# Kernel optimization log

Measured on AMD Instinct MI355X. Metric: run time of the kernel, lower is better.

The kernel has to match this reference:

```python
import jax, jax.numpy as jnp
import numpy as np

T, B, I, H = 256, 128, 512, 1024

def setup_inputs() -> dict:
    key = jax.random.key(0)
    k1, k2, k3, k4, k5 = jax.random.split(key, 5)
    s_ih = 1.0 / np.sqrt(H)
    return {
        "x": jax.random.normal(k1, (T, B, I), dtype=jnp.float32),
        "hidden": jnp.zeros((B, H), dtype=jnp.float32),
        "W_ih": jax.random.uniform(k2, (H, I), jnp.float32, -s_ih, s_ih),
        "W_hh": jax.random.uniform(k3, (H, H), jnp.float32, -s_ih, s_ih),
        "b_ih": jax.random.uniform(k4, (H,), jnp.float32, -s_ih, s_ih),
        "b_hh": jax.random.uniform(k5, (H,), jnp.float32, -s_ih, s_ih),
    }

def reference(x, hidden, W_ih, W_hh, b_ih, b_hh):
    # Faithful to the source: forward() applies the RNNCell to the SAME
    # initial hidden at every timestep (hidden is never updated in the loop).
    # out[t] = relu(x[t] @ W_ih^T + b_ih + hidden @ W_hh^T + b_hh)
    h_term = hidden @ W_hh.T + b_hh          # (B, H), shared across time
    pre = jnp.einsum('tbi,hi->tbh', x, W_ih) + b_ih + h_term  # (T, B, H)
    out = jax.nn.relu(pre)
    return out, out[-1]
```

## Files before the change

### kernel.cpp

```cpp
#include <hip/hip_runtime.h>
#include <hip/hip_bf16.h>
#include <stdint.h>

#define T_DIM 256
#define B_DIM 128
#define I_DIM 512
#define H_DIM 1024
#define M_DIM (T_DIM * B_DIM)

typedef __attribute__((ext_vector_type(4))) float f32x4;
typedef __attribute__((ext_vector_type(8))) short short8;

__device__ inline unsigned short f2bf(float f) {
    __hip_bfloat16 h = __float2bfloat16(f);
    unsigned short u;
    __builtin_memcpy(&u, &h, sizeof(u));
    return u;
}

__device__ inline void gload_lds16(const void* g, void* l) {
    __builtin_amdgcn_global_load_lds(
        (const __attribute__((address_space(1))) uint32_t*)g,
        (__attribute__((address_space(3))) uint32_t*)l, 16, 0, 0);
}

__global__ void pack_swz(const float* __restrict__ src,
                         unsigned short* __restrict__ dst) {
    int id = blockIdx.x * 256 + threadIdx.x;
    int slot = id & 7;
    int row = (id >> 3) & 127;
    int kst = (id >> 10) & 7;
    int tile = id >> 13;
    int g = slot ^ (row & 7);
    const float* s = src + (size_t)(tile * 128 + row) * I_DIM + kst * 64 + g * 8;
    f32x4 lo = *(const f32x4*)s;
    f32x4 hi = *(const f32x4*)(s + 4);
    union { unsigned short us[8]; short8 v; } pk;
#pragma unroll
    for (int j = 0; j < 4; ++j) { pk.us[j] = f2bf(lo[j]); pk.us[4 + j] = f2bf(hi[j]); }
    *(short8*)(dst + (size_t)id * 8) = pk.v;
}

__global__ __launch_bounds__(256, 2) void gemm_main(
    const unsigned short* __restrict__ Xp, const unsigned short* __restrict__ Wp,
    const float* __restrict__ biasall, float* __restrict__ C,
    float* __restrict__ Clast) {
    __shared__ unsigned short As[2][128 * 64];
    __shared__ unsigned short Bs[2][128 * 64];

    const int tid = threadIdx.x;
    const int lane = tid & 63;
    const int wid = tid >> 6;
    const int wr = wid >> 1, wc = wid & 1;
    const int llo = lane & 15, lhi = lane >> 4;

    const int orig = blockIdx.x;
    const int wg = ((orig & 7) * (2048 >> 3)) + (orig >> 3);
    const int mt = wg >> 3;
    const int nt = wg & 7;
    const int m0 = mt * 128;
    const int n0 = nt * 128;

    const unsigned short* Abase = Xp + (size_t)mt * 65536 + (size_t)tid * 8;
    const unsigned short* Bbase = Wp + (size_t)nt * 65536 + (size_t)tid * 8;

    auto stage = [&](int kst, int buf) {
        const unsigned short* a = Abase + (size_t)kst * 8192;
        const unsigned short* b = Bbase + (size_t)kst * 8192;
#pragma unroll
        for (int g = 0; g < 4; ++g)
            gload_lds16(a + g * 2048, (char*)As[buf] + (g * 256 + tid) * 16);
#pragma unroll
        for (int g = 0; g < 4; ++g)
            gload_lds16(b + g * 2048, (char*)Bs[buf] + (g * 256 + tid) * 16);
    };

    f32x4 acc[4][4] = {};

    auto compute = [&](int buf) {
#pragma unroll
        for (int ks = 0; ks < 2; ++ks) {
            short8 af[4], bfv[4];
#pragma unroll
            for (int mi = 0; mi < 4; ++mi) {
                int ar = wr * 64 + mi * 16 + llo;
                int g = ks * 4 + lhi;
                af[mi] = *(const short8*)&As[buf][ar * 64 + ((g ^ (ar & 7)) << 3)];
            }
#pragma unroll
            for (int ni = 0; ni < 4; ++ni) {
                int br = wc * 64 + ni * 16 + llo;
                int g = ks * 4 + lhi;
                bfv[ni] = *(const short8*)&Bs[buf][br * 64 + ((g ^ (br & 7)) << 3)];
            }
#pragma unroll
            for (int mi = 0; mi < 4; ++mi)
#pragma unroll
                for (int ni = 0; ni < 4; ++ni)
                    acc[mi][ni] = __builtin_amdgcn_mfma_f32_16x16x32_bf16(
                        af[mi], bfv[ni], acc[mi][ni], 0, 0, 0);
        }
    };

    stage(0, 0);
    stage(1, 1);
#pragma unroll
    for (int k = 0; k < 8; ++k) {
        if (k < 7)
            asm volatile("s_waitcnt vmcnt(8)" ::: "memory");
        else
            asm volatile("s_waitcnt vmcnt(0)" ::: "memory");
        __builtin_amdgcn_s_barrier();
        __builtin_amdgcn_sched_barrier(0);
        compute(k & 1);
        __builtin_amdgcn_sched_barrier(0);
        __builtin_amdgcn_s_barrier();
        if (k + 2 < 8) stage(k + 2, k & 1);
    }

    const bool last_tile = (m0 == M_DIM - 128);
#pragma unroll
    for (int mi = 0; mi < 4; ++mi) {
#pragma unroll
        for (int ni = 0; ni < 4; ++ni) {
            int col = n0 + wc * 64 + ni * 16 + llo;
            int rowb = m0 + wr * 64 + mi * 16 + lhi * 4;
#pragma unroll
            for (int r = 0; r < 4; ++r) {
                int row = rowb + r;
                float v = acc[mi][ni][r] + biasall[(row & 127) * H_DIM + col];
                v = fmaxf(v, 0.0f);
                C[(size_t)row * H_DIM + col] = v;
                if (last_tile) Clast[(row & 127) * H_DIM + col] = v;
            }
        }
    }
}

template <int MODE>
__global__ __launch_bounds__(256, 2) void gemm_bt(
    const float* __restrict__ A, const float* __restrict__ Bm,
    int M, int N, int K,
    const float* __restrict__ bias0, const float* __restrict__ bias1,
    float* __restrict__ C, float* __restrict__ Clast) {
    __shared__ unsigned short As[128 * 64];
    __shared__ unsigned short Bs[128 * 64];

    const int tid = threadIdx.x;
    const int wid = tid >> 6;
    const int lane = tid & 63;
    const int wr = wid >> 1, wc = wid & 1;
    const int lhi = lane >> 4;
    const int llo = lane & 15;

    const int orig = blockIdx.x;
    const int nwg = gridDim.x;
    const int wg = (nwg > 8 && (nwg & 7) == 0)
                       ? ((orig & 7) * (nwg >> 3) + (orig >> 3))
                       : orig;
    const int m0 = (wg >> 3) * 128;
    const int n0 = (wg & 7) * 128;

    const int srow = tid >> 3;
    const int c8 = tid & 7;
    const int slot8 = (c8 ^ (srow & 7)) * 8;

    const float* Aptr = A + (size_t)(m0 + srow) * K + c8 * 8;
    const float* Bptr = Bm + (size_t)(n0 + srow) * K + c8 * 8;

    f32x4 pf[2][4][2];

    auto issue = [&](int k0) {
#pragma unroll
        for (int g = 0; g < 4; ++g) {
            const float* pa = Aptr + (size_t)g * 32 * K + k0;
            const float* pb = Bptr + (size_t)g * 32 * K + k0;
            pf[0][g][0] = *(const f32x4*)pa;
            pf[0][g][1] = *(const f32x4*)(pa + 4);
            pf[1][g][0] = *(const f32x4*)pb;
            pf[1][g][1] = *(const f32x4*)(pb + 4);
        }
    };
    auto write_lds = [&]() {
#pragma unroll
        for (int g = 0; g < 4; ++g) {
            union { unsigned short s[8]; short8 v; } pka, pkb;
#pragma unroll
            for (int j = 0; j < 4; ++j) {
                pka.s[j] = f2bf(pf[0][g][0][j]);
                pka.s[4 + j] = f2bf(pf[0][g][1][j]);
                pkb.s[j] = f2bf(pf[1][g][0][j]);
                pkb.s[4 + j] = f2bf(pf[1][g][1][j]);
            }
            *(short8*)&As[(srow + g * 32) * 64 + slot8] = pka.v;
            *(short8*)&Bs[(srow + g * 32) * 64 + slot8] = pkb.v;
        }
    };

    f32x4 acc[4][4] = {};

    auto compute = [&]() {
#pragma unroll
        for (int ks = 0; ks < 2; ++ks) {
            short8 af[4], bfr[4];
#pragma unroll
            for (int mi = 0; mi < 4; ++mi) {
                int ar = wr * 64 + mi * 16 + llo;
                int slot = ((ks << 2) + lhi) ^ (ar & 7);
                af[mi] = *(const short8*)&As[ar * 64 + slot * 8];
            }
#pragma unroll
            for (int ni = 0; ni < 4; ++ni) {
                int br = wc * 64 + ni * 16 + llo;
                int slot = ((ks << 2) + lhi) ^ (br & 7);
                bfr[ni] = *(const short8*)&Bs[br * 64 + slot * 8];
            }
#pragma unroll
            for (int mi = 0; mi < 4; ++mi)
#pragma unroll
                for (int ni = 0; ni < 4; ++ni)
                    acc[mi][ni] = __builtin_amdgcn_mfma_f32_16x16x32_bf16(
                        af[mi], bfr[ni], acc[mi][ni], 0, 0, 0);
        }
    };

    issue(0);
    write_lds();
    __syncthreads();
    for (int k0 = 64; k0 < K; k0 += 64) {
        issue(k0);
        compute();
        __syncthreads();
        write_lds();
        __syncthreads();
    }
    compute();

    const bool last_tile = (m0 == M - 128);
#pragma unroll
    for (int mi = 0; mi < 4; ++mi) {
#pragma unroll
        for (int ni = 0; ni < 4; ++ni) {
            int col = n0 + wc * 64 + ni * 16 + llo;
            int rowb = m0 + wr * 64 + mi * 16 + lhi * 4;
            if (MODE == 0) {
                float bsum = bias0[col] + bias1[col];
#pragma unroll
                for (int r = 0; r < 4; ++r)
                    C[(size_t)(rowb + r) * N + col] = acc[mi][ni][r] + bsum;
            } else {
#pragma unroll
                for (int r = 0; r < 4; ++r) {
                    int row = rowb + r;
                    float v = acc[mi][ni][r] + bias0[(row & 127) * N + col];
                    v = fmaxf(v, 0.0f);
                    C[(size_t)row * N + col] = v;
                    if (last_tile) Clast[(row & 127) * N + col] = v;
                }
            }
        }
    }
}

extern "C" void kernel_launch(void* const* d_in, const int* in_sizes, int n_in,
                              void* d_out, int out_size, void* d_ws, size_t ws_size,
                              hipStream_t stream) {
    const float* x = (const float*)d_in[0];
    const float* hidden = (const float*)d_in[1];
    const float* W_ih = (const float*)d_in[2];
    const float* W_hh = (const float*)d_in[3];
    const float* b_ih = (const float*)d_in[4];
    const float* b_hh = (const float*)d_in[5];

    float* out = (float*)d_out;
    float* out_last = out + (size_t)T_DIM * B_DIM * H_DIM;

    float* biasall = (float*)d_ws;
    unsigned short* Wp = (unsigned short*)((char*)d_ws + 512 * 1024);
    unsigned short* Xp = (unsigned short*)((char*)d_ws + 1536 * 1024);
    const size_t ws_need = 1536 * 1024 + (size_t)M_DIM * I_DIM * 2;

    gemm_bt<0><<<dim3(H_DIM / 128), dim3(256), 0, stream>>>(
        hidden, W_hh, B_DIM, H_DIM, H_DIM, b_ih, b_hh, biasall, nullptr);

    if (ws_size >= ws_need) {
        pack_swz<<<dim3(M_DIM * I_DIM / 8 / 256), dim3(256), 0, stream>>>(x, Xp);
        pack_swz<<<dim3(H_DIM * I_DIM / 8 / 256), dim3(256), 0, stream>>>(W_ih, Wp);
        gemm_main<<<dim3(M_DIM / 128 * (H_DIM / 128)), dim3(256), 0, stream>>>(
            Xp, Wp, biasall, out, out_last);
    } else {
        gemm_bt<1><<<dim3(M_DIM / 128 * (H_DIM / 128)), dim3(256), 0, stream>>>(
            x, W_ih, M_DIM, H_DIM, I_DIM, biasall, nullptr, out, out_last);
    }
}
```

Before: 132.6 us.

## Use 256x256 GEMM tiles with 512 threads, merge packing, and add scalar bias kernel

Result: slower. 177.2 us (+33.6%).

```diff
diff --git a/kernel.cpp b/kernel.cpp
--- a/kernel.cpp
+++ b/kernel.cpp
@@ -24,15 +24,18 @@
         (__attribute__((address_space(3))) uint32_t*)l, 16, 0, 0);
 }
 
-__global__ void pack_swz(const float* __restrict__ src,
-                         unsigned short* __restrict__ dst) {
+__global__ void pack_both(const float* __restrict__ x,
+                          const float* __restrict__ W,
+                          unsigned short* __restrict__ dst) {
     int id = blockIdx.x * 256 + threadIdx.x;
     int slot = id & 7;
     int row = (id >> 3) & 127;
     int kst = (id >> 10) & 7;
     int tile = id >> 13;
     int g = slot ^ (row & 7);
-    const float* s = src + (size_t)(tile * 128 + row) * I_DIM + kst * 64 + g * 8;
+    const float* base = (tile < 256) ? (x + (size_t)tile * 128 * I_DIM)
+                                     : (W + (size_t)(tile - 256) * 128 * I_DIM);
+    const float* s = base + (size_t)row * I_DIM + kst * 64 + g * 8;
     f32x4 lo = *(const f32x4*)s;
     f32x4 hi = *(const f32x4*)(s + 4);
     union { unsigned short us[8]; short8 v; } pk;
@@ -41,107 +44,135 @@
     *(short8*)(dst + (size_t)id * 8) = pk.v;
 }
 
-__global__ __launch_bounds__(256, 2) void gemm_main(
+__global__ __launch_bounds__(256) void bias_dot(
+    const float* __restrict__ hidden, const float* __restrict__ W_hh,
+    const float* __restrict__ b_ih, const float* __restrict__ b_hh,
+    float* __restrict__ biasall) {
+    int id = blockIdx.x * 256 + threadIdx.x;
+    int b = id >> 10, h = id & 1023;
+    const float* hr = hidden + (size_t)b * H_DIM;
+    const float* wr = W_hh + (size_t)h * H_DIM;
+    float s = 0.f;
+#pragma unroll 4
+    for (int k = 0; k < H_DIM; k += 4) {
+        f32x4 a = *(const f32x4*)(hr + k);
+        f32x4 w = *(const f32x4*)(wr + k);
+        s += a[0] * w[0] + a[1] * w[1] + a[2] * w[2] + a[3] * w[3];
+    }
+    biasall[id] = s + b_ih[h] + b_hh[h];
+}
+
+__global__ __launch_bounds__(512, 1) void gemm256(
     const unsigned short* __restrict__ Xp, const unsigned short* __restrict__ Wp,
     const float* __restrict__ biasall, float* __restrict__ C,
     float* __restrict__ Clast) {
-    __shared__ unsigned short As[2][128 * 64];
-    __shared__ unsigned short Bs[2][128 * 64];
+    __shared__ unsigned short As[2][2][8192];
+    __shared__ unsigned short Bs[2][2][8192];
 
     const int tid = threadIdx.x;
     const int lane = tid & 63;
     const int wid = tid >> 6;
-    const int wr = wid >> 1, wc = wid & 1;
+    const int wm = wid >> 2, wn = wid & 3;
     const int llo = lane & 15, lhi = lane >> 4;
 
     const int orig = blockIdx.x;
-    const int wg = ((orig & 7) * (2048 >> 3)) + (orig >> 3);
-    const int mt = wg >> 3;
-    const int nt = wg & 7;
-    const int m0 = mt * 128;
-    const int n0 = nt * 128;
-
-    const unsigned short* Abase = Xp + (size_t)mt * 65536 + (size_t)tid * 8;
-    const unsigned short* Bbase = Wp + (size_t)nt * 65536 + (size_t)tid * 8;
-
-    auto stage = [&](int kst, int buf) {
-        const unsigned short* a = Abase + (size_t)kst * 8192;
-        const unsigned short* b = Bbase + (size_t)kst * 8192;
-#pragma unroll
-        for (int g = 0; g < 4; ++g)
-            gload_lds16(a + g * 2048, (char*)As[buf] + (g * 256 + tid) * 16);
-#pragma unroll
-        for (int g = 0; g < 4; ++g)
-            gload_lds16(b + g * 2048, (char*)Bs[buf] + (g * 256 + tid) * 16);
-    };
-
-    f32x4 acc[4][4] = {};
+    const int wg = (orig & 7) * 64 + (orig >> 3);
+    const int mt = wg >> 2;
+    const int nt = wg & 3;
+    const int m0 = mt * 256;
+    const int n0 = nt * 256;
+
+    const unsigned short* Ab = Xp + (size_t)(2 * mt) * 65536 + (size_t)tid * 8;
+    const unsigned short* Bb = Wp + (size_t)(2 * nt) * 65536 + (size_t)tid * 8;
+
+    auto stage = [&](int kt, int buf) {
+#pragma unroll
+        for (int img = 0; img < 2; ++img)
+#pragma unroll
+            for (int part = 0; part < 2; ++part) {
+                gload_lds16(Ab + (size_t)img * 65536 + kt * 8192 + part * 4096,
+                            (char*)&As[buf][img][0] + part * 8192 + tid * 16);
+                gload_lds16(Bb + (size_t)img * 65536 + kt * 8192 + part * 4096,
+                            (char*)&Bs[buf][img][0] + part * 8192 + tid * 16);
+            }
+    };
+
+    f32x4 acc[8][4] = {};
 
     auto compute = [&](int buf) {
+        __builtin_amdgcn_s_setprio(1);
 #pragma unroll
         for (int ks = 0; ks < 2; ++ks) {
-            short8 af[4], bfv[4];
-#pragma unroll
-            for (int mi = 0; mi < 4; ++mi) {
-                int ar = wr * 64 + mi * 16 + llo;
+            short8 bfv[4];
+#pragma unroll
+            for (int ni = 0; ni < 4; ++ni) {
+                int rB = (wn & 1) * 64 + ni * 16 + llo;
                 int g = ks * 4 + lhi;
-                af[mi] = *(const short8*)&As[buf][ar * 64 + ((g ^ (ar & 7)) << 3)];
-            }
-#pragma unroll
-            for (int ni = 0; ni < 4; ++ni) {
-                int br = wc * 64 + ni * 16 + llo;
-                int g = ks * 4 + lhi;
-                bfv[ni] = *(const short8*)&Bs[buf][br * 64 + ((g ^ (br & 7)) << 3)];
-            }
-#pragma unroll
-            for (int mi = 0; mi < 4; ++mi)
-#pragma unroll
-                for (int ni = 0; ni < 4; ++ni)
-                    acc[mi][ni] = __builtin_amdgcn_mfma_f32_16x16x32_bf16(
-                        af[mi], bfv[ni], acc[mi][ni], 0, 0, 0);
-        }
+                bfv[ni] = *(const short8*)&Bs[buf][wn >> 1]
+                                             [rB * 64 + ((g ^ (rB & 7)) << 3)];
+            }
+#pragma unroll
+            for (int mh = 0; mh < 2; ++mh) {
+                short8 af[4];
+#pragma unroll
+                for (int mi4 = 0; mi4 < 4; ++mi4) {
+                    int r = (mh * 4 + mi4) * 16 + llo;
+                    int g = ks * 4 + lhi;
+                    af[mi4] = *(const short8*)&As[buf][wm]
+                                                 [r * 64 + ((g ^ (r & 7)) << 3)];
+                }
+#pragma unroll
+                for (int mi4 = 0; mi4 < 4; ++mi4)
+#pragma unroll
+                    for (int ni = 0; ni < 4; ++ni)
+                        acc[mh * 4 + mi4][ni] = __builtin_amdgcn_mfma_f32_16x16x32_bf16(
+                            af[mi4], bfv[ni], acc[mh * 4 + mi4][ni], 0, 0, 0);
+            }
+        }
+        __builtin_amdgcn_s_setprio(0);
     };
 
     stage(0, 0);
     stage(1, 1);
 #pragma unroll
-    for (int k = 0; k < 8; ++k) {
-        if (k < 7)
+    for (int kt = 0; kt < 8; ++kt) {
+        const int buf = kt & 1;
+        if (kt < 7)
             asm volatile("s_waitcnt vmcnt(8)" ::: "memory");
         else
             asm volatile("s_waitcnt vmcnt(0)" ::: "memory");
-        __builtin_amdgcn_s_barrier();
+        asm volatile("s_barrier" ::: "memory");
         __builtin_amdgcn_sched_barrier(0);
-        compute(k & 1);
+        compute(buf);
         __builtin_amdgcn_sched_barrier(0);
-        __builtin_amdgcn_s_barrier();
-        if (k + 2 < 8) stage(k + 2, k & 1);
-    }
-
-    const bool last_tile = (m0 == M_DIM - 128);
-#pragma unroll
-    for (int mi = 0; mi < 4; ++mi) {
+        asm volatile("s_barrier" ::: "memory");
+        if (kt + 2 < 8) stage(kt + 2, buf);
+    }
+
+    const bool last_tile = (mt == 127);
+#pragma unroll
+    for (int mi = 0; mi < 8; ++mi) {
 #pragma unroll
         for (int ni = 0; ni < 4; ++ni) {
-            int col = n0 + wc * 64 + ni * 16 + llo;
-            int rowb = m0 + wr * 64 + mi * 16 + lhi * 4;
+            int col = n0 + wn * 64 + ni * 16 + llo;
+            int rowb = m0 + wm * 128 + mi * 16 + lhi * 4;
 #pragma unroll
             for (int r = 0; r < 4; ++r) {
                 int row = rowb + r;
                 float v = acc[mi][ni][r] + biasall[(row & 127) * H_DIM + col];
                 v = fmaxf(v, 0.0f);
                 C[(size_t)row * H_DIM + col] = v;
-                if (last_tile) Clast[(row & 127) * H_DIM + col] = v;
-            }
-        }
-    }
-}
-
-template <int MODE>
+                if (last_tile && row >= M_DIM - 128)
+                    Clast[(row & 127) * H_DIM + col] = v;
+            }
+        }
+    }
+}
+
 __global__ __launch_bounds__(256, 2) void gemm_bt(
     const float* __restrict__ A, const float* __restrict__ Bm,
     int M, int N, int K,
-    const float* __restrict__ bias0, const float* __restrict__ bias1,
+    const float* __restrict__ bias0,
     float* __restrict__ C, float* __restrict__ Clast) {
     __shared__ unsigned short As[128 * 64];
     __shared__ unsigned short Bs[128 * 64];
@@ -243,20 +274,13 @@
         for (int ni = 0; ni < 4; ++ni) {
             int col = n0 + wc * 64 + ni * 16 + llo;
             int rowb = m0 + wr * 64 + mi * 16 + lhi * 4;
-            if (MODE == 0) {
-                float bsum = bias0[col] + bias1[col];
-#pragma unroll
-                for (int r = 0; r < 4; ++r)
-                    C[(size_t)(rowb + r) * N + col] = acc[mi][ni][r] + bsum;
-            } else {
-#pragma unroll
-                for (int r = 0; r < 4; ++r) {
-                    int row = rowb + r;
-                    float v = acc[mi][ni][r] + bias0[(row & 127) * N + col];
-                    v = fmaxf(v, 0.0f);
-                    C[(size_t)row * N + col] = v;
-                    if (last_tile) Clast[(row & 127) * N + col] = v;
-                }
+#pragma unroll
+            for (int r = 0; r < 4; ++r) {
+                int row = rowb + r;
+                float v = acc[mi][ni][r] + bias0[(row & 127) * N + col];
+                v = fmaxf(v, 0.0f);
+                C[(size_t)row * N + col] = v;
+                if (last_tile) Clast[(row & 127) * N + col] = v;
             }
         }
     }
@@ -276,20 +300,17 @@
     float* out_last = out + (size_t)T_DIM * B_DIM * H_DIM;
 
     float* biasall = (float*)d_ws;
-    unsigned short* Wp = (unsigned short*)((char*)d_ws + 512 * 1024);
-    unsigned short* Xp = (unsigned short*)((char*)d_ws + 1536 * 1024);
-    const size_t ws_need = 1536 * 1024 + (size_t)M_DIM * I_DIM * 2;
-
-    gemm_bt<0><<<dim3(H_DIM / 128), dim3(256), 0, stream>>>(
-        hidden, W_hh, B_DIM, H_DIM, H_DIM, b_ih, b_hh, biasall, nullptr);
+    unsigned short* Xp = (unsigned short*)((char*)d_ws + 512 * 1024);
+    unsigned short* Wp = Xp + (size_t)256 * 65536;
+    const size_t ws_need = 512 * 1024 + (size_t)(256 + 8) * 65536 * 2;
+
+    bias_dot<<<dim3(512), dim3(256), 0, stream>>>(hidden, W_hh, b_ih, b_hh, biasall);
 
     if (ws_size >= ws_need) {
-        pack_swz<<<dim3(M_DIM * I_DIM / 8 / 256), dim3(256), 0, stream>>>(x, Xp);
-        pack_swz<<<dim3(H_DIM * I_DIM / 8 / 256), dim3(256), 0, stream>>>(W_ih, Wp);
-        gemm_main<<<dim3(M_DIM / 128 * (H_DIM / 128)), dim3(256), 0, stream>>>(
-            Xp, Wp, biasall, out, out_last);
+        pack_both<<<dim3(264 * 8192 / 256), dim3(256), 0, stream>>>(x, W_ih, Xp);
+        gemm256<<<dim3(512), dim3(512), 0, stream>>>(Xp, Wp, biasall, out, out_last);
     } else {
-        gemm_bt<1><<<dim3(M_DIM / 128 * (H_DIM / 128)), dim3(256), 0, stream>>>(
-            x, W_ih, M_DIM, H_DIM, I_DIM, biasall, nullptr, out, out_last);
-    }
-}
+        gemm_bt<<<dim3(M_DIM / 128 * (H_DIM / 128)), dim3(256), 0, stream>>>(
+            x, W_ih, M_DIM, H_DIM, I_DIM, biasall, out, out_last);
+    }
+}
```
